# Performance work log

Hardware: AMD Instinct MI355X
Metric: run time of the kernel (lower is better)

The kernel has to match this reference:

```python
import jax, jax.numpy as jnp
import numpy as np

E, D, F = 8, 1024, 4096
G = 2048  # tokens per expert


def setup_inputs() -> dict:
    key = jax.random.key(0)
    k1, k2, k3, k4 = jax.random.split(key, 4)
    scale = 1.0 / np.sqrt(D)
    return {
        "routed_in_egD": jax.random.normal(k1, (E * G, D), dtype=jnp.float32),
        "moe_w_in_eD_F": jax.random.normal(k2, (E * D, F), dtype=jnp.float32) * scale,
        "moe_w_swiglu_eD_F": jax.random.normal(k3, (E * D, F), dtype=jnp.float32) * scale,
        "moe_w_out_eF_D": jax.random.normal(k4, (E * F, D), dtype=jnp.float32) * (1.0 / np.sqrt(F)),
    }


def reference(routed_in_egD, moe_w_in_eD_F, moe_w_swiglu_eD_F, moe_w_out_eF_D):
    w_in = moe_w_in_eD_F.reshape(E, D, F)        # [e, D, F]
    w_swiglu = moe_w_swiglu_eD_F.reshape(E, D, F)
    w_out = moe_w_out_eF_D.reshape(E, F, D)      # [e, F, D]
    x = routed_in_egD.reshape(E, -1, D)          # [e, g, D]
    middle = jnp.einsum("egd,edf->egf", x, w_in)
    gate = jnp.einsum("egd,edf->egf", x, w_swiglu)
    hidden = jax.nn.silu(middle) * gate          # fused SwiGLU
    out = jnp.einsum("egf,efd->egd", hidden, w_out)
    return out.reshape(-1, D)
```

## Files before the change

kernel.cpp:

```cpp
#include <hip/hip_runtime.h>
#include <hip/hip_bf16.h>

#define E_ 8
#define D_ 1024
#define F_ 4096
#define G_ 2048

typedef __attribute__((ext_vector_type(8))) short bf16x8;
typedef __attribute__((ext_vector_type(4))) float f32x4;
typedef __attribute__((ext_vector_type(8))) unsigned short u16x8;
typedef unsigned short u16;
typedef unsigned int u32;

#define MFMA_ __builtin_amdgcn_mfma_f32_16x16x32_bf16
#define FENCE() asm volatile("" ::: "memory")
#define BAR()                          \
  do {                                 \
    FENCE();                           \
    __builtin_amdgcn_s_barrier();      \
    FENCE();                           \
  } while (0)

__device__ __forceinline__ u16 f2bf(float f) {
  u32 u = __float_as_uint(f);
  u = (u + 0x7fffu + ((u >> 16) & 1u)) >> 16;
  return (u16)u;
}

__device__ __forceinline__ void gld_lds16(const void* g, void* l) {
  __builtin_amdgcn_global_load_lds(
      (const __attribute__((address_space(1))) u32*)g,
      (__attribute__((address_space(3))) u32*)l, 16, 0, 0);
}

__device__ __forceinline__ void stage_half(const u16* __restrict__ g, int ld,
                                           char* l, int tid) {
  const int wb = (tid & ~63) * 16;
#pragma unroll
  for (int j = 0; j < 2; j++) {
    const int idx = j * 512 + tid;
    const int row = idx >> 3;
    const int grp = (idx & 7) ^ (row & 7);
    gld_lds16(g + (size_t)row * ld + grp * 8, l + j * 8192 + wb);
  }
}

__device__ __forceinline__ bf16x8 ld_frag(const u16* base, int r, int gw) {
  return *(const bf16x8*)(base + r * 64 + ((gw ^ (r & 7)) << 3));
}

__global__ __launch_bounds__(256) void k_cvt(const float* __restrict__ in,
                                             u16* __restrict__ out, int n8) {
  int i = blockIdx.x * 256 + threadIdx.x;
  if (i >= n8) return;
  const float4* p = (const float4*)in + (size_t)i * 2;
  float4 a = p[0], b = p[1];
  u16x8 o;
  o[0] = f2bf(a.x); o[1] = f2bf(a.y); o[2] = f2bf(a.z); o[3] = f2bf(a.w);
  o[4] = f2bf(b.x); o[5] = f2bf(b.y); o[6] = f2bf(b.z); o[7] = f2bf(b.w);
  *(u16x8*)(out + (size_t)i * 8) = o;
}

__global__ __launch_bounds__(256) void k_tcvt(const float* __restrict__ in,
                                              u16* __restrict__ out, int R, int C) {
  __shared__ __align__(16) u16 Tt[64 * 72];
  size_t base = (size_t)blockIdx.z * (size_t)R * (size_t)C;
  in += base; out += base;
  const int c0 = blockIdx.x * 64, r0 = blockIdx.y * 64;
  const int tid = threadIdx.x;
  {
    const int cq = tid & 15, rr = tid >> 4;
    const float* ip = in + (size_t)(r0 + rr) * C + c0 + cq * 4;
#pragma unroll
    for (int i = 0; i < 4; i++) {
      float4 v = *(const float4*)(ip + (size_t)(16 * i) * C);
      const int r = rr + 16 * i, c = cq * 4;
      Tt[(c + 0) * 72 + r] = f2bf(v.x);
      Tt[(c + 1) * 72 + r] = f2bf(v.y);
      Tt[(c + 2) * 72 + r] = f2bf(v.z);
      Tt[(c + 3) * 72 + r] = f2bf(v.w);
    }
  }
  __syncthreads();
  {
    const int rq = tid & 7, cc0 = tid >> 3;
#pragma unroll
    for (int i = 0; i < 2; i++) {
      const int cc = cc0 + 32 * i;
      u16x8 v = *(const u16x8*)(Tt + cc * 72 + rq * 8);
      *(u16x8*)(out + (size_t)(c0 + cc) * R + r0 + rq * 8) = v;
    }
  }
}

__global__ __launch_bounds__(512, 2) void k_mlp1(const u16* __restrict__ X,
                                                 const u16* __restrict__ W1t,
                                                 const u16* __restrict__ W2t,
                                                 u16* __restrict__ H) {
  __shared__ __align__(128) char smem[131072];
  u16* lp = (u16*)smem;
  const int e = blockIdx.z;
  const u16* Ag  = X   + (size_t)e * G_ * D_;
  const u16* B1g = W1t + (size_t)e * F_ * D_;
  const u16* B2g = W2t + (size_t)e * F_ * D_;
  u16* Hp = H + (size_t)e * G_ * F_;
  const int bm = blockIdx.y * 256, bn = blockIdx.x * 128;
  const int tid = threadIdx.x, wave = tid >> 6, lane = tid & 63;
  const int wm = wave >> 1, wn = wave & 1;
  const int quad = lane >> 4, l16 = lane & 15;
  const int NT = D_ / 64;

  f32x4 acc1[4][4], acc2[4][4];
#pragma unroll
  for (int i = 0; i < 4; i++)
#pragma unroll
    for (int j = 0; j < 4; j++) {
      acc1[i][j] = f32x4{0.f, 0.f, 0.f, 0.f};
      acc2[i][j] = f32x4{0.f, 0.f, 0.f, 0.f};
    }

  stage_half(Ag  + (size_t)bm * D_,              D_, smem,                  tid);
  stage_half(Ag  + (size_t)(bm + 128) * D_,      D_, smem + 16384,          tid);
  stage_half(B1g + (size_t)bn * D_,              D_, smem + 32768,          tid);
  stage_half(B2g + (size_t)bn * D_,              D_, smem + 49152,          tid);
  stage_half(B1g + (size_t)bn * D_ + 64,         D_, smem + 65536 + 32768,  tid);
  stage_half(B2g + (size_t)bn * D_ + 64,         D_, smem + 65536 + 49152,  tid);
  asm volatile("s_waitcnt vmcnt(0)" ::: "memory");
  BAR();

  for (int t = 0; t < NT; ++t) {
    const int q = t & 1, qn = q ^ 1;
    const u16* Aw  = lp + q * 32768 + (wm >> 1) * 8192;
    const u16* B1w = lp + q * 32768 + 16384;
    const u16* B2w = lp + q * 32768 + 24576;
    const int ar = (wm & 1) * 64 + l16;
    const int br = wn * 64 + l16;
    bf16x8 afr[4][2], bfr[4][2];

#pragma unroll
    for (int n = 0; n < 4; n++) {
      bfr[n][0] = ld_frag(B1w, br + n * 16, quad);
      bfr[n][1] = ld_frag(B1w, br + n * 16, 4 + quad);
    }
#pragma unroll
    for (int m = 0; m < 2; m++) {
      afr[m][0] = ld_frag(Aw, ar + m * 16, quad);
      afr[m][1] = ld_frag(Aw, ar + m * 16, 4 + quad);
    }
    if (t + 1 < NT)
      stage_half(Ag + (size_t)bm * D_ + (t + 1) * 64, D_, smem + qn * 65536, tid);
    BAR();
    __builtin_amdgcn_s_setprio(1);
#pragma unroll
    for (int m = 0; m < 2; m++)
#pragma unroll
      for (int n = 0; n < 4; n++) {
        acc1[m][n] = MFMA_(afr[m][0], bfr[n][0], acc1[m][n], 0, 0, 0);
        acc1[m][n] = MFMA_(afr[m][1], bfr[n][1], acc1[m][n], 0, 0, 0);
      }
    __builtin_amdgcn_s_setprio(0);
    BAR();

#pragma unroll
    for (int m = 2; m < 4; m++) {
      afr[m][0] = ld_frag(Aw, ar + m * 16, quad);
      afr[m][1] = ld_frag(Aw, ar + m * 16, 4 + quad);
    }
    if (t + 1 < NT)
      stage_half(Ag + (size_t)(bm + 128) * D_ + (t + 1) * 64, D_,
                 smem + qn * 65536 + 16384, tid);
    BAR();
    __builtin_amdgcn_s_setprio(1);
#pragma unroll
    for (int m = 2; m < 4; m++)
#pragma unroll
      for (int n = 0; n < 4; n++) {
        acc1[m][n] = MFMA_(afr[m][0], bfr[n][0], acc1[m][n], 0, 0, 0);
        acc1[m][n] = MFMA_(afr[m][1], bfr[n][1], acc1[m][n], 0, 0, 0);
      }
    __builtin_amdgcn_s_setprio(0);
    BAR();

#pragma unroll
    for (int n = 0; n < 4; n++) {
      bfr[n][0] = ld_frag(B2w, br + n * 16, quad);
      bfr[n][1] = ld_frag(B2w, br + n * 16, 4 + quad);
    }
    if (t + 2 < NT)
      stage_half(B1g + (size_t)bn * D_ + (t + 2) * 64, D_,
                 smem + q * 65536 + 32768, tid);
    BAR();
    __builtin_amdgcn_s_setprio(1);
#pragma unroll
    for (int m = 0; m < 2; m++)
#pragma unroll
      for (int n = 0; n < 4; n++) {
        acc2[m][n] = MFMA_(afr[m][0], bfr[n][0], acc2[m][n], 0, 0, 0);
        acc2[m][n] = MFMA_(afr[m][1], bfr[n][1], acc2[m][n], 0, 0, 0);
      }
    __builtin_amdgcn_s_setprio(0);
    BAR();

    if (t + 2 < NT) {
      stage_half(B2g + (size_t)bn * D_ + (t + 2) * 64, D_,
                 smem + q * 65536 + 49152, tid);
      asm volatile("s_waitcnt vmcnt(4)" ::: "memory");
    } else {
      asm volatile("s_waitcnt vmcnt(0)" ::: "memory");
    }
    BAR();
    __builtin_amdgcn_s_setprio(1);
#pragma unroll
    for (int m = 2; m < 4; m++)
#pragma unroll
      for (int n = 0; n < 4; n++) {
        acc2[m][n] = MFMA_(afr[m][0], bfr[n][0], acc2[m][n], 0, 0, 0);
        acc2[m][n] = MFMA_(afr[m][1], bfr[n][1], acc2[m][n], 0, 0, 0);
      }
    __builtin_amdgcn_s_setprio(0);
    BAR();
  }

#pragma unroll
  for (int m = 0; m < 4; m++)
#pragma unroll
    for (int n = 0; n < 4; n++)
#pragma unroll
      for (int r = 0; r < 4; r++) {
        float mm = acc1[m][n][r], g = acc2[m][n][r];
        float h = (mm / (1.f + __expf(-mm))) * g;
        int row = bm + wm * 64 + m * 16 + quad * 4 + r;
        int col = bn + wn * 64 + n * 16 + l16;
        Hp[(size_t)row * F_ + col] = f2bf(h);
      }
}

__global__ __launch_bounds__(512, 2) void k_mlp2(const u16* __restrict__ H,
                                                 const u16* __restrict__ W3t,
                                                 float* __restrict__ O) {
  __shared__ __align__(128) char smem[131072];
  u16* lp = (u16*)smem;
  const int e = blockIdx.z;
  const u16* Ag = H   + (size_t)e * G_ * F_;
  const u16* Bg = W3t + (size_t)e * D_ * F_;
  float* C = O + (size_t)e * G_ * D_;
  const int bm = blockIdx.y * 256, bn = blockIdx.x * 256;
  const int tid = threadIdx.x, wave = tid >> 6, lane = tid & 63;
  const int wm = wave >> 2, wn = wave & 3;
  const int quad = lane >> 4, l16 = lane & 15;
  const int NT = F_ / 64;

  f32x4 acc[8][4];
#pragma unroll
  for (int i = 0; i < 8; i++)
#pragma unroll
    for (int j = 0; j < 4; j++) acc[i][j] = f32x4{0.f, 0.f, 0.f, 0.f};

  stage_half(Ag + (size_t)bm * F_,               F_, smem,                 tid);
  stage_half(Ag + (size_t)(bm + 128) * F_,       F_, smem + 16384,         tid);
  stage_half(Bg + (size_t)bn * F_,               F_, smem + 32768,         tid);
  stage_half(Bg + (size_t)(bn + 128) * F_,       F_, smem + 49152,         tid);
  stage_half(Bg + (size_t)bn * F_ + 64,          F_, smem + 65536 + 32768, tid);
  stage_half(Bg + (size_t)(bn + 128) * F_ + 64,  F_, smem + 65536 + 49152, tid);
  asm volatile("s_waitcnt vmcnt(0)" ::: "memory");
  BAR();

  for (int t = 0; t < NT; ++t) {
    const int q = t & 1, qn = q ^ 1;
    const u16* Aw = lp + q * 32768 + wm * 8192;
    const u16* Bw = lp + q * 32768 + 16384 + (wn >> 1) * 8192;
    const int br = (wn & 1) * 64 + l16;
    bf16x8 bfr[4][2], a0, a1, a2, a3;

#pragma unroll
    for (int n = 0; n < 4; n++) {
      bfr[n][0] = ld_frag(Bw, br + n * 16, quad);
      bfr[n][1] = ld_frag(Bw, br + n * 16, 4 + quad);
    }
    a0 = ld_frag(Aw, l16, quad);       a1 = ld_frag(Aw, l16, 4 + quad);
    a2 = ld_frag(Aw, 16 + l16, quad);  a3 = ld_frag(Aw, 16 + l16, 4 + quad);
    if (t + 1 < NT)
      stage_half(Ag + (size_t)bm * F_ + (t + 1) * 64, F_, smem + qn * 65536, tid);
    BAR();
    __builtin_amdgcn_s_setprio(1);
#pragma unroll
    for (int n = 0; n < 4; n++) {
      acc[0][n] = MFMA_(a0, bfr[n][0], acc[0][n], 0, 0, 0);
      acc[0][n] = MFMA_(a1, bfr[n][1], acc[0][n], 0, 0, 0);
      acc[1][n] = MFMA_(a2, bfr[n][0], acc[1][n], 0, 0, 0);
      acc[1][n] = MFMA_(a3, bfr[n][1], acc[1][n], 0, 0, 0);
    }
    __builtin_amdgcn_s_setprio(0);
    BAR();

    a0 = ld_frag(Aw, 32 + l16, quad);  a1 = ld_frag(Aw, 32 + l16, 4 + quad);
    a2 = ld_frag(Aw, 48 + l16, quad);  a3 = ld_frag(Aw, 48 + l16, 4 + quad);
    if (t + 1 < NT)
      stage_half(Ag + (size_t)(bm + 128) * F_ + (t + 1) * 64, F_,
                 smem + qn * 65536 + 16384, tid);
    BAR();
    __builtin_amdgcn_s_setprio(1);
#pragma unroll
    for (int n = 0; n < 4; n++) {
      acc[2][n] = MFMA_(a0, bfr[n][0], acc[2][n], 0, 0, 0);
      acc[2][n] = MFMA_(a1, bfr[n][1], acc[2][n], 0, 0, 0);
      acc[3][n] = MFMA_(a2, bfr[n][0], acc[3][n], 0, 0, 0);
      acc[3][n] = MFMA_(a3, bfr[n][1], acc[3][n], 0, 0, 0);
    }
    __builtin_amdgcn_s_setprio(0);
    BAR();

    a0 = ld_frag(Aw, 64 + l16, quad);  a1 = ld_frag(Aw, 64 + l16, 4 + quad);
    a2 = ld_frag(Aw, 80 + l16, quad);  a3 = ld_frag(Aw, 80 + l16, 4 + quad);
    if (t + 2 < NT)
      stage_half(Bg + (size_t)bn * F_ + (t + 2) * 64, F_,
                 smem + q * 65536 + 32768, tid);
    BAR();
    __builtin_amdgcn_s_setprio(1);
#pragma unroll
    for (int n = 0; n < 4; n++) {
      acc[4][n] = MFMA_(a0, bfr[n][0], acc[4][n], 0, 0, 0);
      acc[4][n] = MFMA_(a1, bfr[n][1], acc[4][n], 0, 0, 0);
      acc[5][n] = MFMA_(a2, bfr[n][0], acc[5][n], 0, 0, 0);
      acc[5][n] = MFMA_(a3, bfr[n][1], acc[5][n], 0, 0, 0);
    }
    __builtin_amdgcn_s_setprio(0);
    BAR();

    a0 = ld_frag(Aw, 96 + l16, quad);   a1 = ld_frag(Aw, 96 + l16, 4 + quad);
    a2 = ld_frag(Aw, 112 + l16, quad);  a3 = ld_frag(Aw, 112 + l16, 4 + quad);
    if (t + 2 < NT) {
      stage_half(Bg + (size_t)(bn + 128) * F_ + (t + 2) * 64, F_,
                 smem + q * 65536 + 49152, tid);
      asm volatile("s_waitcnt vmcnt(4)" ::: "memory");
    } else {
      asm volatile("s_waitcnt vmcnt(0)" ::: "memory");
    }
    BAR();
    __builtin_amdgcn_s_setprio(1);
#pragma unroll
    for (int n = 0; n < 4; n++) {
      acc[6][n] = MFMA_(a0, bfr[n][0], acc[6][n], 0, 0, 0);
      acc[6][n] = MFMA_(a1, bfr[n][1], acc[6][n], 0, 0, 0);
      acc[7][n] = MFMA_(a2, bfr[n][0], acc[7][n], 0, 0, 0);
      acc[7][n] = MFMA_(a3, bfr[n][1], acc[7][n], 0, 0, 0);
    }
    __builtin_amdgcn_s_setprio(0);
    BAR();
  }

#pragma unroll
  for (int m = 0; m < 8; m++)
#pragma unroll
    for (int n = 0; n < 4; n++)
#pragma unroll
      for (int r = 0; r < 4; r++) {
        int row = bm + wm * 128 + m * 16 + quad * 4 + r;
        int col = bn + wn * 64 + n * 16 + l16;
        C[(size_t)row * D_ + col] = acc[m][n][r];
      }
}

extern "C" void kernel_launch(void* const* d_in, const int* in_sizes, int n_in,
                              void* d_out, int out_size, void* d_ws, size_t ws_size,
                              hipStream_t stream) {
  const float* x  = (const float*)d_in[0];
  const float* w1 = (const float*)d_in[1];
  const float* w2 = (const float*)d_in[2];
  const float* w3 = (const float*)d_in[3];
  float* out = (float*)d_out;
  char* ws = (char*)d_ws;

  u16* Xb  = (u16*)(ws);
  u16* W1t = (u16*)(ws + (size_t)32 * 1024 * 1024);
  u16* W2t = (u16*)(ws + (size_t)96 * 1024 * 1024);
  u16* Hb  = (u16*)(ws + (size_t)160 * 1024 * 1024);
  u16* W3t = (u16*)(ws);

  k_cvt<<<dim3((E_ * G_ * D_ / 8 + 255) / 256), dim3(256), 0, stream>>>(
      x, Xb, E_ * G_ * D_ / 8);
  k_tcvt<<<dim3(F_ / 64, D_ / 64, E_), dim3(256), 0, stream>>>(w1, W1t, D_, F_);
  k_tcvt<<<dim3(F_ / 64, D_ / 64, E_), dim3(256), 0, stream>>>(w2, W2t, D_, F_);
  k_mlp1<<<dim3(F_ / 128, G_ / 256, E_), dim3(512), 0, stream>>>(Xb, W1t, W2t, Hb);
  k_tcvt<<<dim3(D_ / 64, F_ / 64, E_), dim3(256), 0, stream>>>(w3, W3t, F_, D_);
  k_mlp2<<<dim3(D_ / 256, G_ / 256, E_), dim3(512), 0, stream>>>(Hb, W3t, out);
}
```

Before: 818.4 us.

## Switch GEMMs to 32x32x16 MFMA and make mlp1 blocks loop over N tiles

Both GEMM kernels now use the 32x32x16 bf16 MFMA instruction instead of 16x16x32, which needs fewer fragment loads from LDS per flop. k_mlp1 also becomes persistent along N: each block walks 8 consecutive 128-wide column tiles in one pipelined loop, writing the SwiGLU epilogue after each tile and resetting its accumulators. This keeps the K pipeline running across tiles, but shrinks the grid 8x (256 blocks for mlp1), which may leave compute units underused.

```diff
diff --git a/kernel.cpp b/kernel.cpp
--- a/kernel.cpp
+++ b/kernel.cpp
@@ -8,11 +8,12 @@
 
 typedef __attribute__((ext_vector_type(8))) short bf16x8;
 typedef __attribute__((ext_vector_type(4))) float f32x4;
+typedef __attribute__((ext_vector_type(16))) float f32x16;
 typedef __attribute__((ext_vector_type(8))) unsigned short u16x8;
 typedef unsigned short u16;
 typedef unsigned int u32;
 
-#define MFMA_ __builtin_amdgcn_mfma_f32_16x16x32_bf16
+#define MFMA32 __builtin_amdgcn_mfma_f32_32x32x16_bf16
 #define FENCE() asm volatile("" ::: "memory")
 #define BAR()                          \
   do {                                 \
@@ -104,105 +105,100 @@
   const u16* B1g = W1t + (size_t)e * F_ * D_;
   const u16* B2g = W2t + (size_t)e * F_ * D_;
   u16* Hp = H + (size_t)e * G_ * F_;
-  const int bm = blockIdx.y * 256, bn = blockIdx.x * 128;
+  const int bm = blockIdx.y * 256;
+  const int bn0 = blockIdx.x * 1024;
   const int tid = threadIdx.x, wave = tid >> 6, lane = tid & 63;
   const int wm = wave >> 1, wn = wave & 1;
-  const int quad = lane >> 4, l16 = lane & 15;
-  const int NT = D_ / 64;
-
-  f32x4 acc1[4][4], acc2[4][4];
-#pragma unroll
-  for (int i = 0; i < 4; i++)
-#pragma unroll
-    for (int j = 0; j < 4; j++) {
-      acc1[i][j] = f32x4{0.f, 0.f, 0.f, 0.f};
-      acc2[i][j] = f32x4{0.f, 0.f, 0.f, 0.f};
-    }
-
-  stage_half(Ag  + (size_t)bm * D_,              D_, smem,                  tid);
-  stage_half(Ag  + (size_t)(bm + 128) * D_,      D_, smem + 16384,          tid);
-  stage_half(B1g + (size_t)bn * D_,              D_, smem + 32768,          tid);
-  stage_half(B2g + (size_t)bn * D_,              D_, smem + 49152,          tid);
-  stage_half(B1g + (size_t)bn * D_ + 64,         D_, smem + 65536 + 32768,  tid);
-  stage_half(B2g + (size_t)bn * D_ + 64,         D_, smem + 65536 + 49152,  tid);
+  const int l32 = lane & 31, lhi = lane >> 5;
+  const int NU = 8 * (D_ / 64);
+
+  f32x16 z;
+#pragma unroll
+  for (int i = 0; i < 16; i++) z[i] = 0.f;
+  f32x16 acc1[2][2], acc2[2][2];
+#pragma unroll
+  for (int i = 0; i < 2; i++)
+#pragma unroll
+    for (int j = 0; j < 2; j++) { acc1[i][j] = z; acc2[i][j] = z; }
+
+  const int arb = (wm & 1) * 64;
+  const int brb = wn * 64;
+
+#define KOF(u) (((u) & 15) * 64)
+#define BNF(u) (bn0 + ((u) >> 4) * 128)
+
+  stage_half(Ag  + (size_t)bm * D_,                        D_, smem,                 tid);
+  stage_half(Ag  + (size_t)(bm + 128) * D_,                D_, smem + 16384,         tid);
+  stage_half(B1g + (size_t)BNF(0) * D_,                    D_, smem + 32768,         tid);
+  stage_half(B2g + (size_t)BNF(0) * D_,                    D_, smem + 49152,         tid);
+  stage_half(B1g + (size_t)BNF(1) * D_ + KOF(1),           D_, smem + 65536 + 32768, tid);
+  stage_half(B2g + (size_t)BNF(1) * D_ + KOF(1),           D_, smem + 65536 + 49152, tid);
   asm volatile("s_waitcnt vmcnt(0)" ::: "memory");
   BAR();
 
-  for (int t = 0; t < NT; ++t) {
-    const int q = t & 1, qn = q ^ 1;
+  for (int u = 0; u < NU; ++u) {
+    const int q = u & 1, qn = q ^ 1;
     const u16* Aw  = lp + q * 32768 + (wm >> 1) * 8192;
     const u16* B1w = lp + q * 32768 + 16384;
     const u16* B2w = lp + q * 32768 + 24576;
-    const int ar = (wm & 1) * 64 + l16;
-    const int br = wn * 64 + l16;
-    bf16x8 afr[4][2], bfr[4][2];
-
-#pragma unroll
-    for (int n = 0; n < 4; n++) {
-      bfr[n][0] = ld_frag(B1w, br + n * 16, quad);
-      bfr[n][1] = ld_frag(B1w, br + n * 16, 4 + quad);
-    }
-#pragma unroll
-    for (int m = 0; m < 2; m++) {
-      afr[m][0] = ld_frag(Aw, ar + m * 16, quad);
-      afr[m][1] = ld_frag(Aw, ar + m * 16, 4 + quad);
-    }
-    if (t + 1 < NT)
-      stage_half(Ag + (size_t)bm * D_ + (t + 1) * 64, D_, smem + qn * 65536, tid);
-    BAR();
-    __builtin_amdgcn_s_setprio(1);
-#pragma unroll
-    for (int m = 0; m < 2; m++)
-#pragma unroll
-      for (int n = 0; n < 4; n++) {
-        acc1[m][n] = MFMA_(afr[m][0], bfr[n][0], acc1[m][n], 0, 0, 0);
-        acc1[m][n] = MFMA_(afr[m][1], bfr[n][1], acc1[m][n], 0, 0, 0);
-      }
-    __builtin_amdgcn_s_setprio(0);
-    BAR();
-
-#pragma unroll
-    for (int m = 2; m < 4; m++) {
-      afr[m][0] = ld_frag(Aw, ar + m * 16, quad);
-      afr[m][1] = ld_frag(Aw, ar + m * 16, 4 + quad);
-    }
-    if (t + 1 < NT)
-      stage_half(Ag + (size_t)(bm + 128) * D_ + (t + 1) * 64, D_,
+    bf16x8 af[2][4], b1f[2][4], b2f[2][4];
+
+#pragma unroll
+    for (int nb = 0; nb < 2; nb++)
+#pragma unroll
+      for (int ks = 0; ks < 4; ks++)
+        b1f[nb][ks] = ld_frag(B1w, brb + nb * 32 + l32, 2 * ks + lhi);
+#pragma unroll
+    for (int ks = 0; ks < 4; ks++)
+      af[0][ks] = ld_frag(Aw, arb + l32, 2 * ks + lhi);
+    if (u + 1 < NU)
+      stage_half(Ag + (size_t)bm * D_ + KOF(u + 1), D_, smem + qn * 65536, tid);
+    BAR();
+    __builtin_amdgcn_s_setprio(1);
+#pragma unroll
+    for (int ks = 0; ks < 4; ks++)
+#pragma unroll
+      for (int nb = 0; nb < 2; nb++)
+        acc1[0][nb] = MFMA32(af[0][ks], b1f[nb][ks], acc1[0][nb], 0, 0, 0);
+    __builtin_amdgcn_s_setprio(0);
+    BAR();
+
+#pragma unroll
+    for (int ks = 0; ks < 4; ks++)
+      af[1][ks] = ld_frag(Aw, arb + 32 + l32, 2 * ks + lhi);
+    if (u + 1 < NU)
+      stage_half(Ag + (size_t)(bm + 128) * D_ + KOF(u + 1), D_,
                  smem + qn * 65536 + 16384, tid);
     BAR();
     __builtin_amdgcn_s_setprio(1);
 #pragma unroll
-    for (int m = 2; m < 4; m++)
-#pragma unroll
-      for (int n = 0; n < 4; n++) {
-        acc1[m][n] = MFMA_(afr[m][0], bfr[n][0], acc1[m][n], 0, 0, 0);
-        acc1[m][n] = MFMA_(afr[m][1], bfr[n][1], acc1[m][n], 0, 0, 0);
-      }
-    __builtin_amdgcn_s_setprio(0);
-    BAR();
-
-#pragma unroll
-    for (int n = 0; n < 4; n++) {
-      bfr[n][0] = ld_frag(B2w, br + n * 16, quad);
-      bfr[n][1] = ld_frag(B2w, br + n * 16, 4 + quad);
-    }
-    if (t + 2 < NT)
-      stage_half(B1g + (size_t)bn * D_ + (t + 2) * 64, D_,
+    for (int ks = 0; ks < 4; ks++)
+#pragma unroll
+      for (int nb = 0; nb < 2; nb++)
+        acc1[1][nb] = MFMA32(af[1][ks], b1f[nb][ks], acc1[1][nb], 0, 0, 0);
+    __builtin_amdgcn_s_setprio(0);
+    BAR();
+
+#pragma unroll
+    for (int nb = 0; nb < 2; nb++)
+#pragma unroll
+      for (int ks = 0; ks < 4; ks++)
+        b2f[nb][ks] = ld_frag(B2w, brb + nb * 32 + l32, 2 * ks + lhi);
+    if (u + 2 < NU)
+      stage_half(B1g + (size_t)BNF(u + 2) * D_ + KOF(u + 2), D_,
                  smem + q * 65536 + 32768, tid);
     BAR();
     __builtin_amdgcn_s_setprio(1);
 #pragma unroll
-    for (int m = 0; m < 2; m++)
-#pragma unroll
-      for (int n = 0; n < 4; n++) {
-        acc2[m][n] = MFMA_(afr[m][0], bfr[n][0], acc2[m][n], 0, 0, 0);
-        acc2[m][n] = MFMA_(afr[m][1], bfr[n][1], acc2[m][n], 0, 0, 0);
-      }
-    __builtin_amdgcn_s_setprio(0);
-    BAR();
-
-    if (t + 2 < NT) {
-      stage_half(B2g + (size_t)bn * D_ + (t + 2) * 64, D_,
+    for (int ks = 0; ks < 4; ks++)
+#pragma unroll
+      for (int nb = 0; nb < 2; nb++)
+        acc2[0][nb] = MFMA32(af[0][ks], b2f[nb][ks], acc2[0][nb], 0, 0, 0);
+    __builtin_amdgcn_s_setprio(0);
+    BAR();
+
+    if (u + 2 < NU) {
+      stage_half(B2g + (size_t)BNF(u + 2) * D_ + KOF(u + 2), D_,
                  smem + q * 65536 + 49152, tid);
       asm volatile("s_waitcnt vmcnt(4)" ::: "memory");
     } else {
@@ -211,28 +207,34 @@
     BAR();
     __builtin_amdgcn_s_setprio(1);
 #pragma unroll
-    for (int m = 2; m < 4; m++)
-#pragma unroll
-      for (int n = 0; n < 4; n++) {
-        acc2[m][n] = MFMA_(afr[m][0], bfr[n][0], acc2[m][n], 0, 0, 0);
-        acc2[m][n] = MFMA_(afr[m][1], bfr[n][1], acc2[m][n], 0, 0, 0);
-      }
-    __builtin_amdgcn_s_setprio(0);
-    BAR();
-  }
-
-#pragma unroll
-  for (int m = 0; m < 4; m++)
-#pragma unroll
-    for (int n = 0; n < 4; n++)
-#pragma unroll
-      for (int r = 0; r < 4; r++) {
-        float mm = acc1[m][n][r], g = acc2[m][n][r];
-        float h = (mm / (1.f + __expf(-mm))) * g;
-        int row = bm + wm * 64 + m * 16 + quad * 4 + r;
-        int col = bn + wn * 64 + n * 16 + l16;
-        Hp[(size_t)row * F_ + col] = f2bf(h);
-      }
+    for (int ks = 0; ks < 4; ks++)
+#pragma unroll
+      for (int nb = 0; nb < 2; nb++)
+        acc2[1][nb] = MFMA32(af[1][ks], b2f[nb][ks], acc2[1][nb], 0, 0, 0);
+    __builtin_amdgcn_s_setprio(0);
+    BAR();
+
+    if ((u & 15) == 15) {
+      const int bn = BNF(u);
+#pragma unroll
+      for (int mb = 0; mb < 2; mb++)
+#pragma unroll
+        for (int nb = 0; nb < 2; nb++) {
+#pragma unroll
+          for (int r = 0; r < 16; r++) {
+            float mm = acc1[mb][nb][r], g = acc2[mb][nb][r];
+            float h = (mm / (1.f + __expf(-mm))) * g;
+            int row = bm + wm * 64 + mb * 32 + (r & 3) + 8 * (r >> 2) + 4 * lhi;
+            int col = bn + wn * 64 + nb * 32 + l32;
+            Hp[(size_t)row * F_ + col] = f2bf(h);
+          }
+          acc1[mb][nb] = z;
+          acc2[mb][nb] = z;
+        }
+    }
+  }
+#undef KOF
+#undef BNF
 }
 
 __global__ __launch_bounds__(512, 2) void k_mlp2(const u16* __restrict__ H,
@@ -247,14 +249,19 @@
   const int bm = blockIdx.y * 256, bn = blockIdx.x * 256;
   const int tid = threadIdx.x, wave = tid >> 6, lane = tid & 63;
   const int wm = wave >> 2, wn = wave & 3;
-  const int quad = lane >> 4, l16 = lane & 15;
+  const int l32 = lane & 31, lhi = lane >> 5;
   const int NT = F_ / 64;
 
-  f32x4 acc[8][4];
-#pragma unroll
-  for (int i = 0; i < 8; i++)
-#pragma unroll
-    for (int j = 0; j < 4; j++) acc[i][j] = f32x4{0.f, 0.f, 0.f, 0.f};
+  f32x16 z;
+#pragma unroll
+  for (int i = 0; i < 16; i++) z[i] = 0.f;
+  f32x16 acc[4][2];
+#pragma unroll
+  for (int i = 0; i < 4; i++)
+#pragma unroll
+    for (int j = 0; j < 2; j++) acc[i][j] = z;
+
+  const int brb = (wn & 1) * 64;
 
   stage_half(Ag + (size_t)bm * F_,               F_, smem,                 tid);
   stage_half(Ag + (size_t)(bm + 128) * F_,       F_, smem + 16384,         tid);
@@ -269,66 +276,63 @@
     const int q = t & 1, qn = q ^ 1;
     const u16* Aw = lp + q * 32768 + wm * 8192;
     const u16* Bw = lp + q * 32768 + 16384 + (wn >> 1) * 8192;
-    const int br = (wn & 1) * 64 + l16;
-    bf16x8 bfr[4][2], a0, a1, a2, a3;
-
-#pragma unroll
-    for (int n = 0; n < 4; n++) {
-      bfr[n][0] = ld_frag(Bw, br + n * 16, quad);
-      bfr[n][1] = ld_frag(Bw, br + n * 16, 4 + quad);
-    }
-    a0 = ld_frag(Aw, l16, quad);       a1 = ld_frag(Aw, l16, 4 + quad);
-    a2 = ld_frag(Aw, 16 + l16, quad);  a3 = ld_frag(Aw, 16 + l16, 4 + quad);
+    bf16x8 bf[2][4], af[4];
+
+#pragma unroll
+    for (int nb = 0; nb < 2; nb++)
+#pragma unroll
+      for (int ks = 0; ks < 4; ks++)
+        bf[nb][ks] = ld_frag(Bw, brb + nb * 32 + l32, 2 * ks + lhi);
+#pragma unroll
+    for (int ks = 0; ks < 4; ks++)
+      af[ks] = ld_frag(Aw, l32, 2 * ks + lhi);
     if (t + 1 < NT)
       stage_half(Ag + (size_t)bm * F_ + (t + 1) * 64, F_, smem + qn * 65536, tid);
     BAR();
     __builtin_amdgcn_s_setprio(1);
 #pragma unroll
-    for (int n = 0; n < 4; n++) {
-      acc[0][n] = MFMA_(a0, bfr[n][0], acc[0][n], 0, 0, 0);
-      acc[0][n] = MFMA_(a1, bfr[n][1], acc[0][n], 0, 0, 0);
-      acc[1][n] = MFMA_(a2, bfr[n][0], acc[1][n], 0, 0, 0);
-      acc[1][n] = MFMA_(a3, bfr[n][1], acc[1][n], 0, 0, 0);
-    }
-    __builtin_amdgcn_s_setprio(0);
-    BAR();
-
-    a0 = ld_frag(Aw, 32 + l16, quad);  a1 = ld_frag(Aw, 32 + l16, 4 + quad);
-    a2 = ld_frag(Aw, 48 + l16, quad);  a3 = ld_frag(Aw, 48 + l16, 4 + quad);
+    for (int ks = 0; ks < 4; ks++)
+#pragma unroll
+      for (int nb = 0; nb < 2; nb++)
+        acc[0][nb] = MFMA32(af[ks], bf[nb][ks], acc[0][nb], 0, 0, 0);
+    __builtin_amdgcn_s_setprio(0);
+    BAR();
+
+#pragma unroll
+    for (int ks = 0; ks < 4; ks++)
+      af[ks] = ld_frag(Aw, 32 + l32, 2 * ks + lhi);
     if (t + 1 < NT)
       stage_half(Ag + (size_t)(bm + 128) * F_ + (t + 1) * 64, F_,
                  smem + qn * 65536 + 16384, tid);
     BAR();
     __builtin_amdgcn_s_setprio(1);
 #pragma unroll
-    for (int n = 0; n < 4; n++) {
-      acc[2][n] = MFMA_(a0, bfr[n][0], acc[2][n], 0, 0, 0);
-      acc[2][n] = MFMA_(a1, bfr[n][1], acc[2][n], 0, 0, 0);
-      acc[3][n] = MFMA_(a2, bfr[n][0], acc[3][n], 0, 0, 0);
-      acc[3][n] = MFMA_(a3, bfr[n][1], acc[3][n], 0, 0, 0);
-    }
-    __builtin_amdgcn_s_setprio(0);
-    BAR();
-
-    a0 = ld_frag(Aw, 64 + l16, quad);  a1 = ld_frag(Aw, 64 + l16, 4 + quad);
-    a2 = ld_frag(Aw, 80 + l16, quad);  a3 = ld_frag(Aw, 80 + l16, 4 + quad);
+    for (int ks = 0; ks < 4; ks++)
+#pragma unroll
+      for (int nb = 0; nb < 2; nb++)
+        acc[1][nb] = MFMA32(af[ks], bf[nb][ks], acc[1][nb], 0, 0, 0);
+    __builtin_amdgcn_s_setprio(0);
+    BAR();
+
+#pragma unroll
+    for (int ks = 0; ks < 4; ks++)
+      af[ks] = ld_frag(Aw, 64 + l32, 2 * ks + lhi);
     if (t + 2 < NT)
       stage_half(Bg + (size_t)bn * F_ + (t + 2) * 64, F_,
                  smem + q * 65536 + 32768, tid);
     BAR();
     __builtin_amdgcn_s_setprio(1);
 #pragma unroll
-    for (int n = 0; n < 4; n++) {
-      acc[4][n] = MFMA_(a0, bfr[n][0], acc[4][n], 0, 0, 0);
-      acc[4][n] = MFMA_(a1, bfr[n][1], acc[4][n], 0, 0, 0);
-      acc[5][n] = MFMA_(a2, bfr[n][0], acc[5][n], 0, 0, 0);
-      acc[5][n] = MFMA_(a3, bfr[n][1], acc[5][n], 0, 0, 0);
-    }
-    __builtin_amdgcn_s_setprio(0);
-    BAR();
-
-    a0 = ld_frag(Aw, 96 + l16, quad);   a1 = ld_frag(Aw, 96 + l16, 4 + quad);
-    a2 = ld_frag(Aw, 112 + l16, quad);  a3 = ld_frag(Aw, 112 + l16, 4 + quad);
+    for (int ks = 0; ks < 4; ks++)
+#pragma unroll
+      for (int nb = 0; nb < 2; nb++)
+        acc[2][nb] = MFMA32(af[ks], bf[nb][ks], acc[2][nb], 0, 0, 0);
+    __builtin_amdgcn_s_setprio(0);
+    BAR();
+
+#pragma unroll
+    for (int ks = 0; ks < 4; ks++)
+      af[ks] = ld_frag(Aw, 96 + l32, 2 * ks + lhi);
     if (t + 2 < NT) {
       stage_half(Bg + (size_t)(bn + 128) * F_ + (t + 2) * 64, F_,
                  smem + q * 65536 + 49152, tid);
@@ -339,25 +343,23 @@
     BAR();
     __builtin_amdgcn_s_setprio(1);
 #pragma unroll
-    for (int n = 0; n < 4; n++) {
-      acc[6][n] = MFMA_(a0, bfr[n][0], acc[6][n], 0, 0, 0);
-      acc[6][n] = MFMA_(a1, bfr[n][1], acc[6][n], 0, 0, 0);
-      acc[7][n] = MFMA_(a2, bfr[n][0], acc[7][n], 0, 0, 0);
-      acc[7][n] = MFMA_(a3, bfr[n][1], acc[7][n], 0, 0, 0);
-    }
-    __builtin_amdgcn_s_setprio(0);
-    BAR();
-  }
-
-#pragma unroll
-  for (int m = 0; m < 8; m++)
-#pragma unroll
-    for (int n = 0; n < 4; n++)
-#pragma unroll
-      for (int r = 0; r < 4; r++) {
-        int row = bm + wm * 128 + m * 16 + quad * 4 + r;
-        int col = bn + wn * 64 + n * 16 + l16;
-        C[(size_t)row * D_ + col] = acc[m][n][r];
+    for (int ks = 0; ks < 4; ks++)
+#pragma unroll
+      for (int nb = 0; nb < 2; nb++)
+        acc[3][nb] = MFMA32(af[ks], bf[nb][ks], acc[3][nb], 0, 0, 0);
+    __builtin_amdgcn_s_setprio(0);
+    BAR();
+  }
+
+#pragma unroll
+  for (int mb = 0; mb < 4; mb++)
+#pragma unroll
+    for (int nb = 0; nb < 2; nb++)
+#pragma unroll
+      for (int r = 0; r < 16; r++) {
+        int row = bm + wm * 128 + mb * 32 + (r & 3) + 8 * (r >> 2) + 4 * lhi;
+        int col = bn + wn * 64 + nb * 32 + l32;
+        C[(size_t)row * D_ + col] = acc[mb][nb][r];
       }
 }
 
@@ -381,7 +383,7 @@
       x, Xb, E_ * G_ * D_ / 8);
   k_tcvt<<<dim3(F_ / 64, D_ / 64, E_), dim3(256), 0, stream>>>(w1, W1t, D_, F_);
   k_tcvt<<<dim3(F_ / 64, D_ / 64, E_), dim3(256), 0, stream>>>(w2, W2t, D_, F_);
-  k_mlp1<<<dim3(F_ / 128, G_ / 256, E_), dim3(512), 0, stream>>>(Xb, W1t, W2t, Hb);
+  k_mlp1<<<dim3(F_ / 128 / 8, G_ / 256, E_), dim3(512), 0, stream>>>(Xb, W1t, W2t, Hb);
   k_tcvt<<<dim3(D_ / 64, F_ / 64, E_), dim3(256), 0, stream>>>(w3, W3t, F_, D_);
   k_mlp2<<<dim3(D_ / 256, G_ / 256, E_), dim3(512), 0, stream>>>(Hb, W3t, out);
 }
```

Result: slower. 885.0 us (+8.1%).
